# Kernel tuning notes

Measured on AMD Instinct MI355X. Metric: run time of the kernel, lower is better.

The kernel has to match this reference:

```python
import jax, jax.numpy as jnp
import numpy as np
import math

N, CH, T, S = 32, 64, 2048, 77  # batch*heads, per-head channels, query len, encoder len

def setup_inputs() -> dict:
    key = jax.random.key(0)
    k1, k2 = jax.random.split(key)
    qkv = jax.random.normal(k1, (N, 3 * CH, T), dtype=jnp.float32)
    encoder_kv = jax.random.normal(k2, (N, 2 * CH, S), dtype=jnp.float32)
    attn_mask = jnp.zeros((1, T, S + T), dtype=jnp.float32)
    return {"qkv": qkv, "encoder_kv": encoder_kv, "attn_mask": attn_mask}

def reference(qkv, encoder_kv, attn_mask):
    ch = qkv.shape[1] // 3
    q, k, v = jnp.split(qkv, 3, axis=1)          # each [N, ch, T]
    ek, ev = jnp.split(encoder_kv, 2, axis=1)    # each [N, ch, S]
    k = jnp.concatenate([ek, k], axis=-1)        # [N, ch, S+T]
    v = jnp.concatenate([ev, v], axis=-1)
    scale = 1.0 / math.sqrt(math.sqrt(ch))
    weight = jnp.einsum('bct,bcs->bts', q * scale, k * scale)  # [N, T, S+T]
    weight = weight.astype(jnp.float32) + attn_mask
    weight = jax.nn.softmax(weight, axis=-1).astype(v.dtype)
    return jnp.einsum('bts,bcs->bct', weight, v)  # [N, ch, T]
```

## Files before the change

kernel.cpp:

```cpp
#include <hip/hip_runtime.h>


typedef __attribute__((ext_vector_type(8))) __bf16 bf16x8;
typedef __attribute__((ext_vector_type(8))) unsigned short u16x8;
typedef __attribute__((ext_vector_type(4))) float f32x4;
typedef float f32x4a __attribute__((ext_vector_type(4))) __attribute__((aligned(4)));
typedef __attribute__((ext_vector_type(4))) unsigned u32x4;
typedef __attribute__((ext_vector_type(2))) unsigned u32x2;

#define L2E  1.44269504089f
#define NEGM (-23.0830936f)

static __device__ __forceinline__ unsigned short f2bf(float f) {
    unsigned u = __builtin_bit_cast(unsigned, f);
    u += 0x7fffu + ((u >> 16) & 1u);
    return (unsigned short)(u >> 16);
}

static __device__ __forceinline__ unsigned pack_bf16(float a, float b) {
#if __has_builtin(__builtin_amdgcn_cvt_pk_bf16_f32)
    typedef __bf16 bf16x2_t __attribute__((ext_vector_type(2)));
    bf16x2_t r = __builtin_amdgcn_cvt_pk_bf16_f32(a, b);
    unsigned u; __builtin_memcpy(&u, &r, 4);
    return u;
#else
    unsigned ua = __builtin_bit_cast(unsigned, a);
    unsigned ub = __builtin_bit_cast(unsigned, b);
    ua += 0x7fffu + ((ua >> 16) & 1u);
    ub += 0x7fffu + ((ub >> 16) & 1u);
    return __builtin_amdgcn_perm(ub, ua, 0x07060302u);
#endif
}

__global__ __launch_bounds__(256) void prep_all(const float* __restrict__ qkv,
                                                const float* __restrict__ ekv,
                                                unsigned short* __restrict__ kws,
                                                unsigned short* __restrict__ vws) {
    int b = blockIdx.x;
    int tid = threadIdx.x;

    if (b >= 1088) {
        int bb = b - 1088;
        int n = bb >> 6, c = bb & 63;
        const float* v  = qkv + (size_t)n * 192 * 2048 + (size_t)(128 + c) * 2048;
        const float* ev = ekv + (size_t)n * 128 * 77 + (size_t)(64 + c) * 77;
        unsigned short* dst = vws + ((size_t)n * 64 + c) * 2176;
        for (int u = tid; u < 544; u += 256) {
            int s = u << 2;
            float f[4];
            if (u >= 20 && u <= 530) {
                f32x4a x = *(const f32x4a*)(v + s - 77);
                f[0] = x.x; f[1] = x.y; f[2] = x.z; f[3] = x.w;
            } else {
                #pragma unroll
                for (int k = 0; k < 4; ++k) {
                    int sk = s + k;
                    f[k] = (sk < 77) ? ev[sk] : ((sk < 2125) ? v[sk - 77] : 0.f);
                }
            }
            u32x2 pk; pk.x = pack_bf16(f[0], f[1]); pk.y = pack_bf16(f[2], f[3]);
            *(u32x2*)(dst + s) = pk;
        }
        return;
    }

    __shared__ float tile[64][65];
    int mode, n, t0;
    if (b < 1024) { mode = 1; n = b >> 5;          t0 = (b & 31) << 6; }
    else          { mode = 2; n = (b - 1024) >> 1; t0 = ((b - 1024) & 1) << 6; }

    const float* src;
    size_t srow;
    int tmax = 64;
    if (mode == 1) { src = qkv + (size_t)n * 192 * 2048 + (size_t)64 * 2048 + t0; srow = 2048; }
    else           { src = ekv + (size_t)n * 128 * 77 + t0; srow = 77;
                     tmax = 77 - t0; if (tmax > 64) tmax = 64; }

    #pragma unroll
    for (int i = 0; i < 4; ++i) {
        int idx = tid + (i << 8);
        int c  = idx >> 4;
        int t4 = (idx & 15) << 2;
        const float* p = src + (size_t)c * srow + t4;
        float v0, v1, v2, v3;
        if (mode == 1) {
            f32x4 v = *(const f32x4*)p;
            v0 = v.x; v1 = v.y; v2 = v.z; v3 = v.w;
        } else {
            v0 = (t4 + 0 < tmax) ? p[0] : 0.f;
            v1 = (t4 + 1 < tmax) ? p[1] : 0.f;
            v2 = (t4 + 2 < tmax) ? p[2] : 0.f;
            v3 = (t4 + 3 < tmax) ? p[3] : 0.f;
        }
        tile[t4 + 0][c] = v0;
        tile[t4 + 1][c] = v1;
        tile[t4 + 2][c] = v2;
        tile[t4 + 3][c] = v3;
    }
    __syncthreads();
    #pragma unroll
    for (int i = 0; i < 4; ++i) {
        int idx = tid + (i << 8);
        int row = idx >> 4;
        int c4  = (idx & 15) << 2;
        if (mode == 2 && row >= tmax) continue;
        u32x2 pk;
        pk.x = pack_bf16(tile[row][c4 + 0], tile[row][c4 + 1]);
        pk.y = pack_bf16(tile[row][c4 + 2], tile[row][c4 + 3]);
        unsigned short* dst;
        if (mode == 1) dst = kws + ((size_t)n * 2176 + 77 + t0 + row) * 64;
        else           dst = kws + ((size_t)n * 2176 + t0 + row) * 64;
        *(u32x2*)(dst + c4) = pk;
    }
}

__global__ __launch_bounds__(256, 2) void flash_attn(
        const float* __restrict__ qkv,
        const unsigned short* __restrict__ kws,
        const unsigned short* __restrict__ vws,
        const float* __restrict__ mask,
        float* __restrict__ out) {
    __shared__ alignas(16) unsigned short k_lds[2][64 * 72];
    __shared__ alignas(16) unsigned short v_lds[2][64 * 72];
    __shared__ alignas(16) unsigned short p_lds[4][32 * 72];

    const int n    = blockIdx.y;
    const int t0   = blockIdx.x << 7;
    const int tid  = threadIdx.x;
    const int wave = tid >> 6;
    const int lane = tid & 63;
    const int q    = lane >> 4;
    const int l16  = lane & 15;
    const int tc0  = t0 + (wave << 5) + l16;
    const int tc1  = tc0 + 16;

    bf16x8 qf[2][2];
    #pragma unroll
    for (int h = 0; h < 2; ++h) {
        const float* qsrc = qkv + (size_t)n * 192 * 2048 + (h ? tc1 : tc0);
        u16x8 a0, a1;
        #pragma unroll
        for (int j = 0; j < 8; ++j) {
            a0[j] = f2bf(qsrc[(size_t)((q << 3) + j) * 2048] * 0.125f);
            a1[j] = f2bf(qsrc[(size_t)(32 + (q << 3) + j) * 2048] * 0.125f);
        }
        qf[h][0] = __builtin_bit_cast(bf16x8, a0);
        qf[h][1] = __builtin_bit_cast(bf16x8, a1);
    }

    const unsigned short* kg = kws + (size_t)n * 2176 * 64;
    const unsigned short* vg = vws + (size_t)n * 64 * 2176;
    const float* mrow0 = mask + (size_t)tc0 * 2125;
    const float* mrow1 = mask + (size_t)tc1 * 2125;
    unsigned short* const pw0 = p_lds[wave] + (size_t)l16 * 72;
    unsigned short* const pw1 = p_lds[wave] + (size_t)(16 + l16) * 72;

    const int srow0 = tid >> 3,        sch = (tid & 7) << 3;
    const int srow1 = (tid + 256) >> 3;

    f32x4 of[2][4] = {};
    float lsum0 = 0.f, lsum1 = 0.f;

    u32x4 kreg[2], vreg[2];
    f32x4 mreg[4][2];

    auto issue_kv = [&](int s0) {
        kreg[0] = *(const u32x4*)(kg + (size_t)(s0 + srow0) * 64 + sch);
        vreg[0] = *(const u32x4*)(vg + (size_t)srow0 * 2176 + s0 + sch);
        kreg[1] = *(const u32x4*)(kg + (size_t)(s0 + srow1) * 64 + sch);
        vreg[1] = *(const u32x4*)(vg + (size_t)srow1 * 2176 + s0 + sch);
    };
    auto issue_mask = [&](int s0) {
        #pragma unroll
        for (int sm = 0; sm < 4; ++sm) {
            int sbase = s0 + (sm << 4) + (q << 2);
            int sclamp = sbase > 2121 ? 2121 : sbase;
            f32x4a m0 = *(const f32x4a*)(mrow0 + sclamp);
            f32x4a m1 = *(const f32x4a*)(mrow1 + sclamp);
            mreg[sm][0] = f32x4{m0.x, m0.y, m0.z, m0.w};
            mreg[sm][1] = f32x4{m1.x, m1.y, m1.z, m1.w};
        }
    };

    issue_kv(0);
    issue_mask(0);

    for (int ks = 0; ks < 34; ++ks) {
        const int s0 = ks << 6;
        unsigned short* const kb = k_lds[ks & 1];
        unsigned short* const vb = v_lds[ks & 1];
        *(u32x4*)(kb + srow0 * 72 + sch) = kreg[0];
        *(u32x4*)(vb + srow0 * 72 + sch) = vreg[0];
        *(u32x4*)(kb + srow1 * 72 + sch) = kreg[1];
        *(u32x4*)(vb + srow1 * 72 + sch) = vreg[1];
        __syncthreads();
        if (ks < 33) issue_kv(s0 + 64);

        const bool tail = (s0 + 64 > 2125);
        #pragma unroll
        for (int sm = 0; sm < 4; ++sm) {
            const unsigned short* kp = kb + (size_t)((sm << 4) + l16) * 72 + (q << 3);
            bf16x8 ak0 = *(const bf16x8*)(kp);
            bf16x8 ak1 = *(const bf16x8*)(kp + 32);
            int sbase = s0 + (sm << 4) + (q << 2);
            #pragma unroll
            for (int h = 0; h < 2; ++h) {
                f32x4 acc = {};
                acc = __builtin_amdgcn_mfma_f32_16x16x32_bf16(ak0, qf[h][0], acc, 0, 0, 0);
                acc = __builtin_amdgcn_mfma_f32_16x16x32_bf16(ak1, qf[h][1], acc, 0, 0, 0);
                acc += mreg[sm][h];
                if (tail) {
                    #pragma unroll
                    for (int j = 0; j < 4; ++j)
                        if (sbase + j >= 2125) acc[j] = -1e30f;
                }
                float p0 = __builtin_amdgcn_exp2f(__builtin_fmaf(acc[0], L2E, NEGM));
                float p1 = __builtin_amdgcn_exp2f(__builtin_fmaf(acc[1], L2E, NEGM));
                float p2 = __builtin_amdgcn_exp2f(__builtin_fmaf(acc[2], L2E, NEGM));
                float p3 = __builtin_amdgcn_exp2f(__builtin_fmaf(acc[3], L2E, NEGM));
                if (h) lsum1 += (p0 + p1) + (p2 + p3);
                else   lsum0 += (p0 + p1) + (p2 + p3);
                u32x2 pk; pk.x = pack_bf16(p0, p1); pk.y = pack_bf16(p2, p3);
                *(u32x2*)((h ? pw1 : pw0) + (sm << 4) + (q << 2)) = pk;
            }
        }
        if (ks < 33) issue_mask(s0 + 64);

        bf16x8 bp00 = *(const bf16x8*)(pw0 + (q << 3));
        bf16x8 bp01 = *(const bf16x8*)(pw0 + (q << 3) + 32);
        bf16x8 bp10 = *(const bf16x8*)(pw1 + (q << 3));
        bf16x8 bp11 = *(const bf16x8*)(pw1 + (q << 3) + 32);
        #pragma unroll
        for (int cm = 0; cm < 4; ++cm) {
            const unsigned short* vp = vb + (size_t)((cm << 4) + l16) * 72 + (q << 3);
            bf16x8 av0 = *(const bf16x8*)(vp);
            bf16x8 av1 = *(const bf16x8*)(vp + 32);
            of[0][cm] = __builtin_amdgcn_mfma_f32_16x16x32_bf16(av0, bp00, of[0][cm], 0, 0, 0);
            of[0][cm] = __builtin_amdgcn_mfma_f32_16x16x32_bf16(av1, bp01, of[0][cm], 0, 0, 0);
            of[1][cm] = __builtin_amdgcn_mfma_f32_16x16x32_bf16(av0, bp10, of[1][cm], 0, 0, 0);
            of[1][cm] = __builtin_amdgcn_mfma_f32_16x16x32_bf16(av1, bp11, of[1][cm], 0, 0, 0);
        }
    }

    lsum0 += __shfl_xor(lsum0, 16, 64);
    lsum0 += __shfl_xor(lsum0, 32, 64);
    lsum1 += __shfl_xor(lsum1, 16, 64);
    lsum1 += __shfl_xor(lsum1, 32, 64);
    float inv0 = 1.0f / lsum0, inv1 = 1.0f / lsum1;
    #pragma unroll
    for (int cm = 0; cm < 4; ++cm)
        #pragma unroll
        for (int j = 0; j < 4; ++j) {
            int c = (cm << 4) + (q << 2) + j;
            float* o = out + ((size_t)n * 64 + c) * 2048;
            o[tc0] = of[0][cm][j] * inv0;
            o[tc1] = of[1][cm][j] * inv1;
        }
}

extern "C" void kernel_launch(void* const* d_in, const int* in_sizes, int n_in,
                              void* d_out, int out_size, void* d_ws, size_t ws_size,
                              hipStream_t stream) {
    const float* qkv  = (const float*)d_in[0];
    const float* ekv  = (const float*)d_in[1];
    const float* mask = (const float*)d_in[2];
    float* out = (float*)d_out;

    unsigned short* kws = (unsigned short*)d_ws;
    unsigned short* vws = kws + (size_t)32 * 2176 * 64;

    prep_all<<<3136, 256, 0, stream>>>(qkv, ekv, kws, vws);
    dim3 grid(16, 32);
    flash_attn<<<grid, 256, 0, stream>>>(qkv, kws, vws, mask, out);
}
```

Before: 173.8 us.

## Split key sequence across two wave groups and read V directly from global

Doubles the block to 512 threads. Each half of the waves processes half of the key/value sequence for the same 128 queries, and the two partial outputs and row sums are combined through LDS at the end. V tiles are no longer staged in LDS; the second MFMA reads its V fragments directly from global memory. The aim is more parallelism for the small 512-block grid on a 256-CU device. The cost is uncached global V loads in the inner loop, a larger register and LDS footprint per block, and an extra reduction step.

```diff
diff --git a/kernel.cpp b/kernel.cpp
--- a/kernel.cpp
+++ b/kernel.cpp
@@ -114,25 +114,27 @@
     }
 }
 
-__global__ __launch_bounds__(256, 2) void flash_attn(
+__global__ __launch_bounds__(512, 4) void flash_attn(
         const float* __restrict__ qkv,
         const unsigned short* __restrict__ kws,
         const unsigned short* __restrict__ vws,
         const float* __restrict__ mask,
         float* __restrict__ out) {
-    __shared__ alignas(16) unsigned short k_lds[2][64 * 72];
-    __shared__ alignas(16) unsigned short v_lds[2][64 * 72];
-    __shared__ alignas(16) unsigned short p_lds[4][32 * 72];
+    __shared__ alignas(16) unsigned short k_lds[2][2][64 * 72];
+    __shared__ alignas(16) unsigned short p_lds[8][32 * 72];
 
     const int n    = blockIdx.y;
     const int t0   = blockIdx.x << 7;
     const int tid  = threadIdx.x;
     const int wave = tid >> 6;
+    const int h2   = wave >> 2;
+    const int wv   = wave & 3;
     const int lane = tid & 63;
     const int q    = lane >> 4;
     const int l16  = lane & 15;
-    const int tc0  = t0 + (wave << 5) + l16;
+    const int tc0  = t0 + (wv << 5) + l16;
     const int tc1  = tc0 + 16;
+    const int sb   = h2 * 1088;
 
     bf16x8 qf[2][2];
     #pragma unroll
@@ -155,20 +157,19 @@
     unsigned short* const pw0 = p_lds[wave] + (size_t)l16 * 72;
     unsigned short* const pw1 = p_lds[wave] + (size_t)(16 + l16) * 72;
 
-    const int srow0 = tid >> 3,        sch = (tid & 7) << 3;
-    const int srow1 = (tid + 256) >> 3;
+    const int tid256 = tid & 255;
+    const int srow0 = tid256 >> 3, sch = (tid256 & 7) << 3;
+    const int srow1 = srow0 + 32;
 
     f32x4 of[2][4] = {};
     float lsum0 = 0.f, lsum1 = 0.f;
 
-    u32x4 kreg[2], vreg[2];
+    u32x4 kreg[2];
     f32x4 mreg[4][2];
 
-    auto issue_kv = [&](int s0) {
+    auto issue_k = [&](int s0) {
         kreg[0] = *(const u32x4*)(kg + (size_t)(s0 + srow0) * 64 + sch);
-        vreg[0] = *(const u32x4*)(vg + (size_t)srow0 * 2176 + s0 + sch);
         kreg[1] = *(const u32x4*)(kg + (size_t)(s0 + srow1) * 64 + sch);
-        vreg[1] = *(const u32x4*)(vg + (size_t)srow1 * 2176 + s0 + sch);
     };
     auto issue_mask = [&](int s0) {
         #pragma unroll
@@ -182,19 +183,16 @@
         }
     };
 
-    issue_kv(0);
-    issue_mask(0);
-
-    for (int ks = 0; ks < 34; ++ks) {
-        const int s0 = ks << 6;
-        unsigned short* const kb = k_lds[ks & 1];
-        unsigned short* const vb = v_lds[ks & 1];
+    issue_k(sb);
+    issue_mask(sb);
+
+    for (int ks = 0; ks < 17; ++ks) {
+        const int s0 = sb + (ks << 6);
+        unsigned short* const kb = k_lds[h2][ks & 1];
         *(u32x4*)(kb + srow0 * 72 + sch) = kreg[0];
-        *(u32x4*)(vb + srow0 * 72 + sch) = vreg[0];
         *(u32x4*)(kb + srow1 * 72 + sch) = kreg[1];
-        *(u32x4*)(vb + srow1 * 72 + sch) = vreg[1];
         __syncthreads();
-        if (ks < 33) issue_kv(s0 + 64);
+        if (ks < 16) issue_k(s0 + 64);
 
         const bool tail = (s0 + 64 > 2125);
         #pragma unroll
@@ -224,7 +222,7 @@
                 *(u32x2*)((h ? pw1 : pw0) + (sm << 4) + (q << 2)) = pk;
             }
         }
-        if (ks < 33) issue_mask(s0 + 64);
+        if (ks < 16) issue_mask(s0 + 64);
 
         bf16x8 bp00 = *(const bf16x8*)(pw0 + (q << 3));
         bf16x8 bp01 = *(const bf16x8*)(pw0 + (q << 3) + 32);
@@ -232,7 +230,7 @@
         bf16x8 bp11 = *(const bf16x8*)(pw1 + (q << 3) + 32);
         #pragma unroll
         for (int cm = 0; cm < 4; ++cm) {
-            const unsigned short* vp = vb + (size_t)((cm << 4) + l16) * 72 + (q << 3);
+            const unsigned short* vp = vg + (size_t)((cm << 4) + l16) * 2176 + s0 + (q << 3);
             bf16x8 av0 = *(const bf16x8*)(vp);
             bf16x8 av1 = *(const bf16x8*)(vp + 32);
             of[0][cm] = __builtin_amdgcn_mfma_f32_16x16x32_bf16(av0, bp00, of[0][cm], 0, 0, 0);
@@ -246,16 +244,41 @@
     lsum0 += __shfl_xor(lsum0, 32, 64);
     lsum1 += __shfl_xor(lsum1, 16, 64);
     lsum1 += __shfl_xor(lsum1, 32, 64);
-    float inv0 = 1.0f / lsum0, inv1 = 1.0f / lsum1;
-    #pragma unroll
-    for (int cm = 0; cm < 4; ++cm)
-        #pragma unroll
-        for (int j = 0; j < 4; ++j) {
-            int c = (cm << 4) + (q << 2) + j;
-            float* o = out + ((size_t)n * 64 + c) * 2048;
-            o[tc0] = of[0][cm][j] * inv0;
-            o[tc1] = of[1][cm][j] * inv1;
-        }
+
+    float* cof  = (float*)(&k_lds[0][0][0]);
+    float* csum = cof + 128 * 68;
+    __syncthreads();
+    if (h2) {
+        #pragma unroll
+        for (int h = 0; h < 2; ++h) {
+            const int tl = (wv << 5) + (h << 4) + l16;
+            #pragma unroll
+            for (int cm = 0; cm < 4; ++cm)
+                *(f32x4*)(cof + (size_t)tl * 68 + (cm << 4) + (q << 2)) = of[h][cm];
+        }
+        if (lane < 16) {
+            csum[(wv << 5) + lane]      = lsum0;
+            csum[(wv << 5) + 16 + lane] = lsum1;
+        }
+    }
+    __syncthreads();
+    if (!h2) {
+        const int tl0 = (wv << 5) + l16, tl1 = tl0 + 16;
+        const float inv0 = 1.0f / (lsum0 + csum[tl0]);
+        const float inv1 = 1.0f / (lsum1 + csum[tl1]);
+        #pragma unroll
+        for (int cm = 0; cm < 4; ++cm) {
+            f32x4 p0 = *(const f32x4*)(cof + (size_t)tl0 * 68 + (cm << 4) + (q << 2));
+            f32x4 p1 = *(const f32x4*)(cof + (size_t)tl1 * 68 + (cm << 4) + (q << 2));
+            #pragma unroll
+            for (int j = 0; j < 4; ++j) {
+                int c = (cm << 4) + (q << 2) + j;
+                float* o = out + ((size_t)n * 64 + c) * 2048;
+                o[tc0] = (of[0][cm][j] + p0[j]) * inv0;
+                o[tc1] = (of[1][cm][j] + p1[j]) * inv1;
+            }
+        }
+    }
 }
 
 extern "C" void kernel_launch(void* const* d_in, const int* in_sizes, int n_in,
@@ -271,5 +294,5 @@
 
     prep_all<<<3136, 256, 0, stream>>>(qkv, ekv, kws, vws);
     dim3 grid(16, 32);
-    flash_attn<<<grid, 256, 0, stream>>>(qkv, kws, vws, mask, out);
-}
+    flash_attn<<<grid, 512, 0, stream>>>(qkv, kws, vws, mask, out);
+}
```

After: 275.2 us. +58.3%, slower.

## Skip all-zero mask loads via prep-time check and pipeline QK with PV

Applied to the files above, without the earlier changes.

Extra blocks in the prep kernel scan the whole attention mask and set a flag in workspace if any element is nonzero. The attention kernel reads the flag and skips all mask loads and adds when it is clear. The main loop is also restructured so the QK^T MFMAs for the next key tile overlap with the PV MFMAs for the previous tile, using a triple-buffered V shared-memory area. In exchange it adds a memset, a full scan of the mask each call, more shared memory and more registers.

```diff
diff --git a/kernel.cpp b/kernel.cpp
--- a/kernel.cpp
+++ b/kernel.cpp
@@ -35,9 +35,22 @@
 __global__ __launch_bounds__(256) void prep_all(const float* __restrict__ qkv,
                                                 const float* __restrict__ ekv,
                                                 unsigned short* __restrict__ kws,
-                                                unsigned short* __restrict__ vws) {
+                                                unsigned short* __restrict__ vws,
+                                                const float* __restrict__ mask) {
     int b = blockIdx.x;
     int tid = threadIdx.x;
+
+    if (b >= 3136) {
+        int bb = b - 3136;
+        const u32x4* m4 = (const u32x4*)mask;
+        unsigned acc = 0;
+        for (int i = (bb << 8) + tid; i < 1088000; i += 131072) {
+            u32x4 x = m4[i];
+            acc |= x.x | x.y | x.z | x.w;
+        }
+        if (acc) atomicOr((unsigned*)(kws + (size_t)2175 * 64), 1u);
+        return;
+    }
 
     if (b >= 1088) {
         int bb = b - 1088;
@@ -121,7 +134,7 @@
         const float* __restrict__ mask,
         float* __restrict__ out) {
     __shared__ alignas(16) unsigned short k_lds[2][64 * 72];
-    __shared__ alignas(16) unsigned short v_lds[2][64 * 72];
+    __shared__ alignas(16) unsigned short v_lds[3][64 * 72];
     __shared__ alignas(16) unsigned short p_lds[4][32 * 72];
 
     const int n    = blockIdx.y;
@@ -134,6 +147,9 @@
     const int tc0  = t0 + (wave << 5) + l16;
     const int tc1  = tc0 + 16;
 
+    const bool domask =
+        __builtin_amdgcn_readfirstlane(*(const unsigned*)(kws + (size_t)2175 * 64)) != 0u;
+
     bf16x8 qf[2][2];
     #pragma unroll
     for (int h = 0; h < 2; ++h) {
@@ -156,9 +172,10 @@
     unsigned short* const pw1 = p_lds[wave] + (size_t)(16 + l16) * 72;
 
     const int srow0 = tid >> 3,        sch = (tid & 7) << 3;
-    const int srow1 = (tid + 256) >> 3;
+    const int srow1 = srow0 + 32;
 
     f32x4 of[2][4] = {};
+    f32x4 sacc[4][2];
     float lsum0 = 0.f, lsum1 = 0.f;
 
     u32x4 kreg[2], vreg[2];
@@ -181,51 +198,53 @@
             mreg[sm][1] = f32x4{m1.x, m1.y, m1.z, m1.w};
         }
     };
-
-    issue_kv(0);
-    issue_mask(0);
-
-    for (int ks = 0; ks < 34; ++ks) {
-        const int s0 = ks << 6;
-        unsigned short* const kb = k_lds[ks & 1];
-        unsigned short* const vb = v_lds[ks & 1];
+    auto stage = [&](unsigned short* kb, unsigned short* vb) {
         *(u32x4*)(kb + srow0 * 72 + sch) = kreg[0];
         *(u32x4*)(vb + srow0 * 72 + sch) = vreg[0];
         *(u32x4*)(kb + srow1 * 72 + sch) = kreg[1];
         *(u32x4*)(vb + srow1 * 72 + sch) = vreg[1];
-        __syncthreads();
-        if (ks < 33) issue_kv(s0 + 64);
-
-        const bool tail = (s0 + 64 > 2125);
+    };
+    auto qkm = [&](const unsigned short* kb) {
         #pragma unroll
         for (int sm = 0; sm < 4; ++sm) {
             const unsigned short* kp = kb + (size_t)((sm << 4) + l16) * 72 + (q << 3);
             bf16x8 ak0 = *(const bf16x8*)(kp);
             bf16x8 ak1 = *(const bf16x8*)(kp + 32);
+            #pragma unroll
+            for (int h = 0; h < 2; ++h) {
+                f32x4 a = {};
+                a = __builtin_amdgcn_mfma_f32_16x16x32_bf16(ak0, qf[h][0], a, 0, 0, 0);
+                a = __builtin_amdgcn_mfma_f32_16x16x32_bf16(ak1, qf[h][1], a, 0, 0, 0);
+                sacc[sm][h] = a;
+            }
+        }
+    };
+    auto smax = [&](int s0) {
+        const bool tail = (s0 + 64 > 2125);
+        #pragma unroll
+        for (int sm = 0; sm < 4; ++sm) {
             int sbase = s0 + (sm << 4) + (q << 2);
             #pragma unroll
             for (int h = 0; h < 2; ++h) {
-                f32x4 acc = {};
-                acc = __builtin_amdgcn_mfma_f32_16x16x32_bf16(ak0, qf[h][0], acc, 0, 0, 0);
-                acc = __builtin_amdgcn_mfma_f32_16x16x32_bf16(ak1, qf[h][1], acc, 0, 0, 0);
-                acc += mreg[sm][h];
+                f32x4 a = sacc[sm][h];
+                if (domask) a += mreg[sm][h];
                 if (tail) {
                     #pragma unroll
                     for (int j = 0; j < 4; ++j)
-                        if (sbase + j >= 2125) acc[j] = -1e30f;
+                        if (sbase + j >= 2125) a[j] = -1e30f;
                 }
-                float p0 = __builtin_amdgcn_exp2f(__builtin_fmaf(acc[0], L2E, NEGM));
-                float p1 = __builtin_amdgcn_exp2f(__builtin_fmaf(acc[1], L2E, NEGM));
-                float p2 = __builtin_amdgcn_exp2f(__builtin_fmaf(acc[2], L2E, NEGM));
-                float p3 = __builtin_amdgcn_exp2f(__builtin_fmaf(acc[3], L2E, NEGM));
+                float p0 = __builtin_amdgcn_exp2f(__builtin_fmaf(a[0], L2E, NEGM));
+                float p1 = __builtin_amdgcn_exp2f(__builtin_fmaf(a[1], L2E, NEGM));
+                float p2 = __builtin_amdgcn_exp2f(__builtin_fmaf(a[2], L2E, NEGM));
+                float p3 = __builtin_amdgcn_exp2f(__builtin_fmaf(a[3], L2E, NEGM));
                 if (h) lsum1 += (p0 + p1) + (p2 + p3);
                 else   lsum0 += (p0 + p1) + (p2 + p3);
                 u32x2 pk; pk.x = pack_bf16(p0, p1); pk.y = pack_bf16(p2, p3);
                 *(u32x2*)((h ? pw1 : pw0) + (sm << 4) + (q << 2)) = pk;
             }
         }
-        if (ks < 33) issue_mask(s0 + 64);
-
+    };
+    auto pv = [&](const unsigned short* vb) {
         bf16x8 bp00 = *(const bf16x8*)(pw0 + (q << 3));
         bf16x8 bp01 = *(const bf16x8*)(pw0 + (q << 3) + 32);
         bf16x8 bp10 = *(const bf16x8*)(pw1 + (q << 3));
@@ -240,7 +259,31 @@
             of[1][cm] = __builtin_amdgcn_mfma_f32_16x16x32_bf16(av0, bp10, of[1][cm], 0, 0, 0);
             of[1][cm] = __builtin_amdgcn_mfma_f32_16x16x32_bf16(av1, bp11, of[1][cm], 0, 0, 0);
         }
-    }
+    };
+
+    issue_kv(0);
+    if (domask) issue_mask(0);
+    stage(k_lds[0], v_lds[0]);
+    __syncthreads();
+    issue_kv(64);
+    qkm(k_lds[0]);
+    smax(0);
+    if (domask) issue_mask(64);
+
+    int vri = 0, vwi = 1;
+    for (int ks = 0; ks < 33; ++ks) {
+        const int s1 = (ks + 1) << 6;
+        stage(k_lds[(ks + 1) & 1], v_lds[vwi]);
+        __syncthreads();
+        if (ks < 32) issue_kv(s1 + 64);
+        qkm(k_lds[(ks + 1) & 1]);
+        pv(v_lds[vri]);
+        smax(s1);
+        if (domask && ks < 32) issue_mask(s1 + 64);
+        vri = (vri == 2) ? 0 : vri + 1;
+        vwi = (vwi == 2) ? 0 : vwi + 1;
+    }
+    pv(v_lds[vri]);
 
     lsum0 += __shfl_xor(lsum0, 16, 64);
     lsum0 += __shfl_xor(lsum0, 32, 64);
@@ -269,7 +312,8 @@
     unsigned short* kws = (unsigned short*)d_ws;
     unsigned short* vws = kws + (size_t)32 * 2176 * 64;
 
-    prep_all<<<3136, 256, 0, stream>>>(qkv, ekv, kws, vws);
+    hipMemsetAsync((char*)d_ws + (size_t)2175 * 64 * 2, 0, 4, stream);
+    prep_all<<<3648, 256, 0, stream>>>(qkv, ekv, kws, vws, mask);
     dim3 grid(16, 32);
     flash_attn<<<grid, 256, 0, stream>>>(qkv, kws, vws, mask, out);
 }
```

New measurement: 163.0 us. 6.2% less time.
